# Kernel optimization log

Measured on AMD Instinct MI355X. Metric: run time of the kernel, lower is better.

Reference implementation:

```python
import jax, jax.numpy as jnp
import numpy as np

L, N, S, V, D = 4, 32, 2048, 512, 512  # layers, batch, seq, input_dim, hidden


def setup_inputs() -> dict:
    key = jax.random.key(0)
    ks = jax.random.split(key, 5)
    scale_x = 1.0 / np.sqrt(V)
    scale_h = 1.0 / np.sqrt(D)
    return {
        "x": jax.random.normal(ks[0], (N, S, V), dtype=jnp.float32),
        "Wx": jax.random.uniform(ks[1], (L, D, V), dtype=jnp.float32, minval=-scale_x, maxval=scale_x),
        "bx": jax.random.uniform(ks[2], (L, D), dtype=jnp.float32, minval=-scale_x, maxval=scale_x),
        "Wh": jax.random.uniform(ks[3], (L, D, D), dtype=jnp.float32, minval=-scale_h, maxval=scale_h),
        "bh": jax.random.uniform(ks[4], (L, D), dtype=jnp.float32, minval=-scale_h, maxval=scale_h),
    }


def reference(x, Wx, bx, Wh, bh):
    # Each of the L layers independently consumes the raw input x[t] plus its own
    # previous-timestep hidden: h_l[t] = sigmoid(Wx_l x[t] + bx_l + Wh_l h_l[t-1] + bh_l).
    n, s, v = x.shape
    l, d, _ = Wx.shape
    # Batched x-projection for all timesteps/layers up front: [S, L, N, D]
    xp = jnp.einsum('nsv,ldv->slnd', x, Wx) + (bx + bh)[None, :, None, :]
    h0 = jnp.zeros((l, n, d), dtype=x.dtype)

    def step(h, xp_t):
        # h: [L, N, D]; recurrent update fused across layers
        h_new = jax.nn.sigmoid(xp_t + jnp.einsum('lnd,led->lne', h, Wh))
        return h_new, h_new[-1]

    h_final, ys = jax.lax.scan(step, h0, xp)  # ys: [S, N, D]
    final_ans = jnp.transpose(ys, (1, 0, 2))  # [N, S, D]
    return final_ans, h_final
```

## Files before the change

### kernel.cpp

```cpp
#include <hip/hip_runtime.h>

typedef unsigned short u16;
typedef unsigned int u32;
typedef unsigned long long u64;
typedef __attribute__((ext_vector_type(8))) short bf16x8;
typedef __attribute__((ext_vector_type(4))) float f32x4;

#define LL 4
#define NN 32
#define SS 2048
#define VV 512
#define DD 512
#define CHUNK 16
#define NCHUNKS (SS / CHUNK)
#define PADR 520

#define NCONS 8
#define NBLOCKS 256
#define FGROUPS 4
#define NCOMBOS 32
#define CRES 7
#define NPROD_ACTIVE (NCOMBOS * CRES)

#define PRODCNT_OFF 0
#define CONSDONE_OFF (NCONS * NCHUNKS * 4)
#define RING_OFF 8192
#define SLOT_BYTES ((size_t)NCONS * CHUNK * 8 * 64 * 32)

#define LDS_BYTES (131072 + 16 * PADR * 2)

static __device__ __forceinline__ u16 f2bf(float f) {
    u32 x = __float_as_uint(f);
    x += 0x7fffu + ((x >> 16) & 1u);
    return (u16)(x >> 16);
}
static __device__ __forceinline__ float bf2f(u32 h) {
    return __uint_as_float((h & 0xffffu) << 16);
}
static __device__ __forceinline__ bf16x8 cvt8(const float* p) {
    f32x4 a = *(const f32x4*)p;
    f32x4 b = *(const f32x4*)(p + 4);
    bf16x8 r;
    r[0] = (short)f2bf(a[0]); r[1] = (short)f2bf(a[1]);
    r[2] = (short)f2bf(a[2]); r[3] = (short)f2bf(a[3]);
    r[4] = (short)f2bf(b[0]); r[5] = (short)f2bf(b[1]);
    r[6] = (short)f2bf(b[2]); r[7] = (short)f2bf(b[3]);
    return r;
}
static __device__ __forceinline__ float sigmoid_fast(float x) {
    const float e = __builtin_amdgcn_exp2f(x * -1.44269504089f);
    return __builtin_amdgcn_rcpf(1.0f + e);
}

static __device__ __forceinline__ void lds_barrier() {
    asm volatile("s_waitcnt lgkmcnt(0)" ::: "memory");
    __builtin_amdgcn_sched_barrier(0);
    __builtin_amdgcn_s_barrier();
    __builtin_amdgcn_sched_barrier(0);
}

__global__ __launch_bounds__(512, 2) void rnn_fused(
    const float* __restrict__ x,
    const float* __restrict__ Wx,
    const float* __restrict__ bx,
    const float* __restrict__ Wh,
    const float* __restrict__ bh,
    float* __restrict__ out,
    char* __restrict__ ws, int nslots)
{
    extern __shared__ __align__(16) char lds[];
    const int tid = threadIdx.x;
    const int lane = tid & 63;
    const int w = tid >> 6;
    const int col = lane & 15, quad = lane >> 4;
    u32* prod_cnt = (u32*)(ws + PRODCNT_OFF);
    u32* cons_done = (u32*)(ws + CONSDONE_OFF);
    char* ring = ws + RING_OFF;

    if (blockIdx.x < NCONS) {
        const int cl = blockIdx.x;
        const int layer = cl >> 1, nb = cl & 1;
        u16* whlds = (u16*)lds;
        u16* hb = (u16*)(lds + 131072);

        bf16x8 whf[48];
#pragma unroll
        for (int tl = 0; tl < 3; ++tl)
#pragma unroll
            for (int ks = 0; ks < 16; ++ks)
                whf[tl * 16 + ks] =
                    cvt8(Wh + ((size_t)layer * DD + (w * 64 + tl * 16 + col)) * DD + 32 * ks + quad * 8);
#pragma unroll
        for (int ks = 0; ks < 16; ++ks) {
            bf16x8 f = cvt8(Wh + ((size_t)layer * DD + (w * 64 + 48 + col)) * DD + 32 * ks + quad * 8);
            *(bf16x8*)(whlds + ((size_t)(w * 16 + ks) * 64 + lane) * 8) = f;
        }
        for (int i = tid; i < 16 * PADR; i += 512) hb[i] = 0;
        __syncthreads();

        auto xp_addr = [&](int t) -> const u64* {
            const int slot = (t >> 4) % nslots;
            return (const u64*)(ring +
                ((((size_t)(slot * NCONS + cl) * CHUNK + (t & 15)) * 8 + w) * 64 + lane) * 32);
        };
        while (__hip_atomic_load(&prod_cnt[cl * NCHUNKS + 0], __ATOMIC_ACQUIRE,
                                 __HIP_MEMORY_SCOPE_AGENT) < FGROUPS)
            __builtin_amdgcn_s_sleep(8);
        u64 xpbuf[2][4];
        {
            const u64* p = xp_addr(0);
#pragma unroll
            for (int j = 0; j < 4; ++j)
                xpbuf[0][j] = __hip_atomic_load(p + j, __ATOMIC_RELAXED, __HIP_MEMORY_SCOPE_AGENT);
        }

        const u16* hrd = hb + col * PADR + quad * 8;
        const u16* b3b = whlds + (size_t)w * 16 * 64 * 8;
        u16* hwr = hb + (quad * 4) * PADR + w * 64 + col;
        float* outp = out + ((size_t)(nb * 16 + quad * 4) * SS) * DD + w * 64 + col;
        float* out2 = out + (size_t)NN * SS * DD
                    + ((size_t)layer * NN + nb * 16 + quad * 4) * DD + w * 64 + col;

        for (int t = 0; t < SS; ++t) {
            const int cur = t & 1;
            if ((t & 15) == 15) {
                if (tid == 0)
                    __hip_atomic_store(&cons_done[cl * 32], (u32)((t >> 4) + 1),
                                       __ATOMIC_RELEASE, __HIP_MEMORY_SCOPE_AGENT);
            }
            if (t + 1 < SS) {
                if (((t + 1) & 15) == 0) {
                    const int nc = (t + 1) >> 4;
                    while (__hip_atomic_load(&prod_cnt[cl * NCHUNKS + nc], __ATOMIC_ACQUIRE,
                                             __HIP_MEMORY_SCOPE_AGENT) < FGROUPS)
                        __builtin_amdgcn_s_sleep(8);
                }
                const u64* p = xp_addr(t + 1);
#pragma unroll
                for (int j = 0; j < 4; ++j)
                    xpbuf[cur ^ 1][j] =
                        __hip_atomic_load(p + j, __ATOMIC_RELAXED, __HIP_MEMORY_SCOPE_AGENT);
            }
            f32x4 acc[4];
#pragma unroll
            for (int tl = 0; tl < 4; ++tl) {
                const u64 v = xpbuf[cur][tl];
                acc[tl][0] = bf2f((u32)v);
                acc[tl][1] = bf2f((u32)(v >> 16));
                acc[tl][2] = bf2f((u32)(v >> 32));
                acc[tl][3] = bf2f((u32)(v >> 48));
            }
            {
                bf16x8 a0 = *(const bf16x8*)(hrd);
                bf16x8 b0 = *(const bf16x8*)(b3b + lane * 8);
                bf16x8 a1 = *(const bf16x8*)(hrd + 32);
                bf16x8 b1 = *(const bf16x8*)(b3b + 512 + lane * 8);
#pragma unroll
                for (int ks = 0; ks < 16; ++ks) {
                    bf16x8 an = a1, bn = b1;
                    if (ks < 14) {
                        an = *(const bf16x8*)(hrd + 32 * (ks + 2));
                        bn = *(const bf16x8*)(b3b + 512 * (ks + 2) + lane * 8);
                    }
                    acc[0] = __builtin_amdgcn_mfma_f32_16x16x32_bf16(a0, whf[ks], acc[0], 0, 0, 0);
                    acc[1] = __builtin_amdgcn_mfma_f32_16x16x32_bf16(a0, whf[16 + ks], acc[1], 0, 0, 0);
                    acc[2] = __builtin_amdgcn_mfma_f32_16x16x32_bf16(a0, whf[32 + ks], acc[2], 0, 0, 0);
                    acc[3] = __builtin_amdgcn_mfma_f32_16x16x32_bf16(a0, b0, acc[3], 0, 0, 0);
                    a0 = a1; b0 = b1; a1 = an; b1 = bn;
                }
            }
            lds_barrier();
#pragma unroll
            for (int tl = 0; tl < 4; ++tl)
#pragma unroll
                for (int i = 0; i < 4; ++i) {
                    const float s = sigmoid_fast(acc[tl][i]);
                    hwr[i * PADR + tl * 16] = f2bf(s);
                    if (layer == 3) outp[((size_t)i * SS + t) * DD + tl * 16] = s;
                    if (t == SS - 1) out2[(size_t)i * DD + tl * 16] = s;
                }
            if ((t & 15) == 14) __syncthreads();
            else                lds_barrier();
        }
    } else {
        const int q = blockIdx.x - NCONS;
        if (q >= NPROD_ACTIVE) return;
        const int combo = q & 31;
        const int cl = combo >> 2, fg = combo & 3;
        const int layer = cl >> 1, nb = cl & 1;
        u16* blds = (u16*)lds;

        for (int r = 0; r < 16; ++r) {
            const int li = (r * 512 + tid) * 8;
            const int row = li >> 9, k0 = li & 511;
            bf16x8 v = cvt8(Wx + ((size_t)layer * DD + fg * 128 + row) * VV + k0);
            const int ct = row >> 4, fcol = row & 15, ks = k0 >> 5, qd = (k0 >> 3) & 3;
            *(bf16x8*)(blds + ((size_t)((ct * 16 + ks) * 64 + qd * 16 + fcol)) * 8) = v;
        }
        float bias[8];
#pragma unroll
        for (int ct = 0; ct < 8; ++ct) {
            const int f = layer * DD + fg * 128 + ct * 16 + col;
            bias[ct] = bx[f] + bh[f];
        }
        __syncthreads();

        for (int chunk = q >> 5; chunk < NCHUNKS; chunk += CRES) {
            const int t0 = chunk * CHUNK;
            f32x4 acc[2][8];
#pragma unroll
            for (int rt = 0; rt < 2; ++rt)
#pragma unroll
                for (int ct = 0; ct < 8; ++ct)
                    acc[rt][ct] = f32x4{bias[ct], bias[ct], bias[ct], bias[ct]};
            const float* xr0 = x + ((size_t)(nb * 16 + col) * SS + (t0 + 2 * w)) * VV + quad * 8;
#pragma unroll
            for (int ks = 0; ks < 16; ++ks) {
                bf16x8 a0 = cvt8(xr0 + 32 * ks);
                bf16x8 a1 = cvt8(xr0 + VV + 32 * ks);
#pragma unroll
                for (int ct = 0; ct < 8; ++ct) {
                    bf16x8 b = *(const bf16x8*)(blds + ((size_t)((ct * 16 + ks) * 64 + lane)) * 8);
                    acc[0][ct] = __builtin_amdgcn_mfma_f32_16x16x32_bf16(a0, b, acc[0][ct], 0, 0, 0);
                    acc[1][ct] = __builtin_amdgcn_mfma_f32_16x16x32_bf16(a1, b, acc[1][ct], 0, 0, 0);
                }
            }
            const int slot = chunk % nslots;
            if (chunk >= nslots && tid == 0) {
                while ((int)__hip_atomic_load(&cons_done[cl * 32], __ATOMIC_ACQUIRE,
                                              __HIP_MEMORY_SCOPE_AGENT) < chunk - nslots + 1)
                    __builtin_amdgcn_s_sleep(127);
            }
            __syncthreads();
#pragma unroll
            for (int rt = 0; rt < 2; ++rt) {
                char* base = ring + ((size_t)(slot * NCONS + cl) * CHUNK + (2 * w + rt)) * (8 * 64 * 32);
#pragma unroll
                for (int ct = 0; ct < 8; ++ct) {
                    const int gct = fg * 8 + ct, wc = gct >> 2, tl = gct & 3;
                    const f32x4 a = acc[rt][ct];
                    u64 v = (u64)f2bf(a[0]) | ((u64)f2bf(a[1]) << 16)
                          | ((u64)f2bf(a[2]) << 32) | ((u64)f2bf(a[3]) << 48);
                    __hip_atomic_store((u64*)(base + ((size_t)wc * 64 + lane) * 32 + tl * 8), v,
                                       __ATOMIC_RELAXED, __HIP_MEMORY_SCOPE_AGENT);
                }
            }
            __syncthreads();
            if (tid == 0)
                __hip_atomic_fetch_add(&prod_cnt[cl * NCHUNKS + chunk], 1u,
                                       __ATOMIC_RELEASE, __HIP_MEMORY_SCOPE_AGENT);
        }
    }
}

extern "C" void kernel_launch(void* const* d_in, const int* in_sizes, int n_in,
                              void* d_out, int out_size, void* d_ws, size_t ws_size,
                              hipStream_t stream) {
    const float* x  = (const float*)d_in[0];
    const float* Wx = (const float*)d_in[1];
    const float* bx = (const float*)d_in[2];
    const float* Wh = (const float*)d_in[3];
    const float* bh = (const float*)d_in[4];
    float* out = (float*)d_out;
    char* ws = (char*)d_ws;

    int nslots = 1;
    if (ws_size > RING_OFF + SLOT_BYTES) {
        size_t n = (ws_size - RING_OFF) / SLOT_BYTES;
        nslots = (int)(n > 8 ? 8 : n);
    }
    hipFuncSetAttribute((const void*)rnn_fused,
                        hipFuncAttributeMaxDynamicSharedMemorySize, LDS_BYTES);
    hipMemsetAsync(ws, 0, RING_OFF, stream);
    rnn_fused<<<dim3(NBLOCKS), dim3(512), LDS_BYTES, stream>>>(x, Wx, bx, Wh, bh, out, ws, nslots);
}
```

Baseline: 7.186 ms.

## Permute hidden-state K layout to pack bf16 writes into 64-bit LDS stores

Changes the hidden-state column layout in LDS so each lane's four output columns (tl=0..3) are contiguous, and permutes the Wh K-ordering to match via a new gather8 loader. The per-step h writeback becomes four 8-byte LDS stores instead of sixteen 2-byte stores. The LDS B-fragment prefetch is also deepened to three stages. The aim is to cut LDS store instructions and latency on the serial recurrent critical path. In exchange, Wh loading becomes strided float2 gathers, a one-time setup cost.

Result: faster. 6.815 ms (-5.2%).

```diff
diff --git a/kernel.cpp b/kernel.cpp
--- a/kernel.cpp
+++ b/kernel.cpp
@@ -45,6 +45,17 @@
     r[2] = (short)f2bf(a[2]); r[3] = (short)f2bf(a[3]);
     r[4] = (short)f2bf(b[0]); r[5] = (short)f2bf(b[1]);
     r[6] = (short)f2bf(b[2]); r[7] = (short)f2bf(b[3]);
+    return r;
+}
+static __device__ __forceinline__ bf16x8 gather8(const float* Wrow, int ks, int quad) {
+    const int base = (ks >> 1) * 64 + (ks & 1) * 8 + quad * 2;
+    bf16x8 r;
+#pragma unroll
+    for (int jj = 0; jj < 4; ++jj) {
+        const float2 v = *(const float2*)(Wrow + base + jj * 16);
+        r[jj]     = (short)f2bf(v.x);
+        r[jj + 4] = (short)f2bf(v.y);
+    }
     return r;
 }
 static __device__ __forceinline__ float sigmoid_fast(float x) {
@@ -89,10 +100,10 @@
 #pragma unroll
             for (int ks = 0; ks < 16; ++ks)
                 whf[tl * 16 + ks] =
-                    cvt8(Wh + ((size_t)layer * DD + (w * 64 + tl * 16 + col)) * DD + 32 * ks + quad * 8);
+                    gather8(Wh + ((size_t)layer * DD + (w * 64 + tl * 16 + col)) * DD, ks, quad);
 #pragma unroll
         for (int ks = 0; ks < 16; ++ks) {
-            bf16x8 f = cvt8(Wh + ((size_t)layer * DD + (w * 64 + 48 + col)) * DD + 32 * ks + quad * 8);
+            bf16x8 f = gather8(Wh + ((size_t)layer * DD + (w * 64 + 48 + col)) * DD, ks, quad);
             *(bf16x8*)(whlds + ((size_t)(w * 16 + ks) * 64 + lane) * 8) = f;
         }
         for (int i = tid; i < 16 * PADR; i += 512) hb[i] = 0;
@@ -116,7 +127,7 @@
 
         const u16* hrd = hb + col * PADR + quad * 8;
         const u16* b3b = whlds + (size_t)w * 16 * 64 * 8;
-        u16* hwr = hb + (quad * 4) * PADR + w * 64 + col;
+        u16* hwr = hb + (quad * 4) * PADR + w * 64 + col * 4;
         float* outp = out + ((size_t)(nb * 16 + quad * 4) * SS) * DD + w * 64 + col;
         float* out2 = out + (size_t)NN * SS * DD
                     + ((size_t)layer * NN + nb * 16 + quad * 4) * DD + w * 64 + col;
@@ -152,33 +163,42 @@
             }
             {
                 bf16x8 a0 = *(const bf16x8*)(hrd);
+                bf16x8 a1 = *(const bf16x8*)(hrd + 32);
                 bf16x8 b0 = *(const bf16x8*)(b3b + lane * 8);
-                bf16x8 a1 = *(const bf16x8*)(hrd + 32);
                 bf16x8 b1 = *(const bf16x8*)(b3b + 512 + lane * 8);
+                bf16x8 b2 = *(const bf16x8*)(b3b + 1024 + lane * 8);
 #pragma unroll
                 for (int ks = 0; ks < 16; ++ks) {
-                    bf16x8 an = a1, bn = b1;
-                    if (ks < 14) {
-                        an = *(const bf16x8*)(hrd + 32 * (ks + 2));
-                        bn = *(const bf16x8*)(b3b + 512 * (ks + 2) + lane * 8);
-                    }
+                    bf16x8 an = a1, bn = b2;
+                    if (ks < 14) an = *(const bf16x8*)(hrd + 32 * (ks + 2));
+                    if (ks < 13) bn = *(const bf16x8*)(b3b + 512 * (ks + 3) + lane * 8);
                     acc[0] = __builtin_amdgcn_mfma_f32_16x16x32_bf16(a0, whf[ks], acc[0], 0, 0, 0);
                     acc[1] = __builtin_amdgcn_mfma_f32_16x16x32_bf16(a0, whf[16 + ks], acc[1], 0, 0, 0);
                     acc[2] = __builtin_amdgcn_mfma_f32_16x16x32_bf16(a0, whf[32 + ks], acc[2], 0, 0, 0);
                     acc[3] = __builtin_amdgcn_mfma_f32_16x16x32_bf16(a0, b0, acc[3], 0, 0, 0);
-                    a0 = a1; b0 = b1; a1 = an; b1 = bn;
+                    a0 = a1; a1 = an;
+                    b0 = b1; b1 = b2; b2 = bn;
                 }
             }
             lds_barrier();
 #pragma unroll
-            for (int tl = 0; tl < 4; ++tl)
-#pragma unroll
-                for (int i = 0; i < 4; ++i) {
-                    const float s = sigmoid_fast(acc[tl][i]);
-                    hwr[i * PADR + tl * 16] = f2bf(s);
-                    if (layer == 3) outp[((size_t)i * SS + t) * DD + tl * 16] = s;
-                    if (t == SS - 1) out2[(size_t)i * DD + tl * 16] = s;
-                }
+            for (int i = 0; i < 4; ++i) {
+                const float s0 = sigmoid_fast(acc[0][i]);
+                const float s1 = sigmoid_fast(acc[1][i]);
+                const float s2 = sigmoid_fast(acc[2][i]);
+                const float s3 = sigmoid_fast(acc[3][i]);
+                const u64 pk = (u64)f2bf(s0) | ((u64)f2bf(s1) << 16)
+                             | ((u64)f2bf(s2) << 32) | ((u64)f2bf(s3) << 48);
+                *(u64*)(hwr + (size_t)i * PADR) = pk;
+                if (layer == 3) {
+                    float* o = outp + ((size_t)i * SS + t) * DD;
+                    o[0] = s0; o[16] = s1; o[32] = s2; o[48] = s3;
+                }
+                if (t == SS - 1) {
+                    float* o2 = out2 + (size_t)i * DD;
+                    o2[0] = s0; o2[16] = s1; o2[32] = s2; o2[48] = s3;
+                }
+            }
             if ((t & 15) == 14) __syncthreads();
             else                lds_barrier();
         }
```
